# Kernel tuning notes

Hardware: AMD Instinct MI355X
Metric: run time of the kernel (lower is better)

The kernel has to match this reference:

```python
import jax, jax.numpy as jnp
import numpy as np

B_, L_, DM, DI, N_, R_ = 8, 2048, 192, 384, 16, 12  # batch, seq, d_model, d_inner, d_state, dt_rank
LN_EPS = 1e-5


def setup_inputs() -> dict:
    key = jax.random.key(0)
    ks = jax.random.split(key, 7)
    x = jax.random.normal(ks[0], (B_, L_, DM), jnp.float32)
    W_in = (jax.random.normal(ks[1], (2 * DI, DM), jnp.float32) * 0.02)
    x_proj_w = (jax.random.normal(ks[2], (R_ + 2 * N_, DI), jnp.float32) * 0.02)
    dt_std = R_ ** (-0.5)
    dt_proj_w = jax.random.uniform(ks[3], (DI, R_), jnp.float32, -dt_std, dt_std)
    # dt bias init: inverse-softplus of dt ~ LogUniform(1e-3, 1e-1)
    dt = jnp.exp(jax.random.uniform(ks[4], (DI,), jnp.float32) * (np.log(0.1) - np.log(0.001)) + np.log(0.001))
    dt = jnp.clip(dt, 1e-4, None)
    dt_proj_b = dt + jnp.log(-jnp.expm1(-dt))
    # A_log init: log(1..N) repeated over d_inner
    A_logs = jnp.log(jnp.tile(jnp.arange(1, N_ + 1, dtype=jnp.float32), (DI, 1)))  # [DI, N]
    Ds = jnp.ones((DI,), jnp.float32)
    ln_gamma = jnp.ones((DI,), jnp.float32)
    ln_beta = jnp.zeros((DI,), jnp.float32)
    W_out = (jax.random.normal(ks[5], (DM, DI), jnp.float32) * 0.02)
    return dict(x=x, W_in=W_in, x_proj_w=x_proj_w, dt_proj_w=dt_proj_w,
                dt_proj_b=dt_proj_b, A_logs=A_logs, Ds=Ds,
                ln_gamma=ln_gamma, ln_beta=ln_beta, W_out=W_out)


def _selective_scan(u, delta, A, Bs, Cs, Ds):
    # u, delta: [B, L, DI]; A: [DI, N]; Bs, Cs: [B, L, N]; Ds: [DI]
    def step(h, inp):
        d_t, u_t, B_t, C_t = inp              # [B,DI], [B,DI], [B,N], [B,N]
        dA = jnp.exp(d_t[..., None] * A)       # [B,DI,N]
        h = dA * h + (d_t * u_t)[..., None] * B_t[:, None, :]
        y_t = jnp.einsum('bdn,bn->bd', h, C_t)
        return h, y_t

    h0 = jnp.zeros((u.shape[0], u.shape[2], A.shape[1]), u.dtype)
    seq = (jnp.moveaxis(delta, 1, 0), jnp.moveaxis(u, 1, 0),
           jnp.moveaxis(Bs, 1, 0), jnp.moveaxis(Cs, 1, 0))
    _, ys = jax.lax.scan(step, h0, seq)        # ys: [L,B,DI]
    return jnp.moveaxis(ys, 0, 1) + Ds * u     # [B,L,DI]


def reference(x, W_in, x_proj_w, dt_proj_w, dt_proj_b, A_logs, Ds, ln_gamma, ln_beta, W_out):
    # in_proj + SiLU, then split into (u, z)  (d_conv <= 1 branch, non-softmax version)
    xz = jax.nn.silu(x @ W_in.T)               # [B,L,2*DI]
    u, z = jnp.split(xz, 2, axis=-1)           # [B,L,DI] each
    # x -> (dt, B, C) projections (K = 1)
    dbl = jnp.einsum('bld,cd->blc', u, x_proj_w)          # [B,L,R+2N]
    dts = dbl[..., :R_] @ dt_proj_w.T                      # [B,L,DI]
    Bs = dbl[..., R_:R_ + N_]                              # [B,L,N]
    Cs = dbl[..., R_ + N_:]                                # [B,L,N]
    delta = jax.nn.softplus(dts + dt_proj_b)               # delta_bias + softplus
    A = -jnp.exp(A_logs)                                   # [DI,N]
    y = _selective_scan(u, delta, A, Bs, Cs, Ds)           # [B,L,DI]
    # out_norm (LayerNorm over d_inner)
    mu = jnp.mean(y, axis=-1, keepdims=True)
    var = jnp.var(y, axis=-1, keepdims=True)
    y = (y - mu) * jax.lax.rsqrt(var + LN_EPS) * ln_gamma + ln_beta
    # gate and out_proj
    y = y * z
    return y @ W_out.T                                     # [B,L,DM]
```

## Files before the change

kernel.cpp:

```cpp
#include <hip/hip_runtime.h>
#include <hip/hip_bf16.h>
#include <math.h>


#define ROWS 16384
#define NCHUNK 64
#define CLEN 32

typedef short bf16x8 __attribute__((ext_vector_type(8)));
typedef float f32x4 __attribute__((ext_vector_type(4)));

__device__ __forceinline__ unsigned short f2bf(float f) {
    unsigned u = __float_as_uint(f);
    return (unsigned short)((u + 0x7fffu + ((u >> 16) & 1u)) >> 16);
}
__device__ __forceinline__ float bf2f(unsigned short h) {
    return __uint_as_float(((unsigned)h) << 16);
}

#define LOG2E 1.44269504088896f

#define LDK 40
__global__ __launch_bounds__(256) void k1_gemm_silu(
    const float* __restrict__ x, const float* __restrict__ Win,
    float* __restrict__ u, float* __restrict__ z)
{
    __shared__ short Ah[128 * LDK];
    __shared__ short Al[128 * LDK];
    __shared__ short Bh[128 * LDK];
    __shared__ short Bl[128 * LDK];
    const int tid = threadIdx.x;
    const int lane = tid & 63;
    const int w = tid >> 6;
    const int wr = w >> 1, wc = w & 1;
    const int bm = blockIdx.x * 128;
    const int bn = blockIdx.y * 128;

    f32x4 acc[4][4];
#pragma unroll
    for (int i = 0; i < 4; ++i)
#pragma unroll
        for (int j = 0; j < 4; ++j) acc[i][j] = (f32x4)0.f;

    const int r16 = lane & 15, q4 = lane >> 4;

    for (int k0 = 0; k0 < 192; k0 += 32) {
#pragma unroll
        for (int i = 0; i < 4; ++i) {
            int p = tid + i * 256;
            int r = p >> 3, k4 = (p & 7) * 4;
            float4 av = *(const float4*)(x + (size_t)(bm + r) * 192 + k0 + k4);
            unsigned short hx = f2bf(av.x), hy = f2bf(av.y), hz = f2bf(av.z), hw = f2bf(av.w);
            unsigned hi0 = (unsigned)hx | ((unsigned)hy << 16);
            unsigned hi1 = (unsigned)hz | ((unsigned)hw << 16);
            unsigned short lx = f2bf(av.x - bf2f(hx)), ly = f2bf(av.y - bf2f(hy));
            unsigned short lz = f2bf(av.z - bf2f(hz)), lw = f2bf(av.w - bf2f(hw));
            unsigned lo0 = (unsigned)lx | ((unsigned)ly << 16);
            unsigned lo1 = (unsigned)lz | ((unsigned)lw << 16);
            int wi = r * (LDK / 2) + (k4 >> 1);
            ((unsigned*)Ah)[wi] = hi0; ((unsigned*)Ah)[wi + 1] = hi1;
            ((unsigned*)Al)[wi] = lo0; ((unsigned*)Al)[wi + 1] = lo1;

            float4 bv = *(const float4*)(Win + (size_t)(bn + r) * 192 + k0 + k4);
            hx = f2bf(bv.x); hy = f2bf(bv.y); hz = f2bf(bv.z); hw = f2bf(bv.w);
            hi0 = (unsigned)hx | ((unsigned)hy << 16);
            hi1 = (unsigned)hz | ((unsigned)hw << 16);
            lx = f2bf(bv.x - bf2f(hx)); ly = f2bf(bv.y - bf2f(hy));
            lz = f2bf(bv.z - bf2f(hz)); lw = f2bf(bv.w - bf2f(hw));
            lo0 = (unsigned)lx | ((unsigned)ly << 16);
            lo1 = (unsigned)lz | ((unsigned)lw << 16);
            ((unsigned*)Bh)[wi] = hi0; ((unsigned*)Bh)[wi + 1] = hi1;
            ((unsigned*)Bl)[wi] = lo0; ((unsigned*)Bl)[wi + 1] = lo1;
        }
        __syncthreads();

        bf16x8 ah[4], al[4];
#pragma unroll
        for (int mt = 0; mt < 4; ++mt) {
            int off = (wr * 64 + mt * 16 + r16) * LDK + q4 * 8;
            ah[mt] = *(const bf16x8*)(Ah + off);
            al[mt] = *(const bf16x8*)(Al + off);
        }
#pragma unroll
        for (int nt = 0; nt < 4; ++nt) {
            int off = (wc * 64 + nt * 16 + r16) * LDK + q4 * 8;
            bf16x8 bh = *(const bf16x8*)(Bh + off);
            bf16x8 bl = *(const bf16x8*)(Bl + off);
#pragma unroll
            for (int mt = 0; mt < 4; ++mt) {
                acc[mt][nt] = __builtin_amdgcn_mfma_f32_16x16x32_bf16(ah[mt], bh, acc[mt][nt], 0, 0, 0);
                acc[mt][nt] = __builtin_amdgcn_mfma_f32_16x16x32_bf16(ah[mt], bl, acc[mt][nt], 0, 0, 0);
                acc[mt][nt] = __builtin_amdgcn_mfma_f32_16x16x32_bf16(al[mt], bh, acc[mt][nt], 0, 0, 0);
            }
        }
        __syncthreads();
    }

    float* dst = (bn < 384) ? u : z;
    const int col0 = (bn < 384) ? bn : (bn - 384);
#pragma unroll
    for (int mt = 0; mt < 4; ++mt) {
#pragma unroll
        for (int nt = 0; nt < 4; ++nt) {
            int col = col0 + wc * 64 + nt * 16 + r16;
#pragma unroll
            for (int r = 0; r < 4; ++r) {
                int row = bm + wr * 64 + mt * 16 + q4 * 4 + r;
                float s = acc[mt][nt][r];
                dst[(size_t)row * 384 + col] = s / (1.f + __expf(-s));
            }
        }
    }
}

__global__ __launch_bounds__(256) void k2_proj(
    const float* __restrict__ u, const float* __restrict__ xpw,
    const float* __restrict__ dtw, const float* __restrict__ dtb,
    float* __restrict__ delta, float* __restrict__ Bso, float* __restrict__ Cso)
{
    __shared__ float As[64 * 68];
    __shared__ float Bs[64 * 53];
    __shared__ float dtwS[384 * 13];
    __shared__ float dblS[64 * 13];
    const int tid = threadIdx.x;
    const int tx = tid & 15, ty = tid >> 4;
    const int row0 = blockIdx.x * 64;

#pragma unroll
    for (int i = 0; i < 5; ++i) {
        int p = tid + i * 256;
        if (p < 1152) {
            int dd = p / 3, q = (p % 3) * 4;
            float4 v = *(const float4*)(dtw + dd * 12 + q);
            dtwS[dd * 13 + q + 0] = v.x;
            dtwS[dd * 13 + q + 1] = v.y;
            dtwS[dd * 13 + q + 2] = v.z;
            dtwS[dd * 13 + q + 3] = v.w;
        }
    }

    float acc[4][3];
#pragma unroll
    for (int i = 0; i < 4; ++i)
#pragma unroll
        for (int g = 0; g < 3; ++g) acc[i][g] = 0.f;

    for (int k0 = 0; k0 < 384; k0 += 64) {
#pragma unroll
        for (int i = 0; i < 4; ++i) {
            int p = tid + i * 256;
            int r = p >> 4, k4 = (p & 15) * 4;
            float4 v = *(const float4*)(u + (size_t)(row0 + r) * 384 + k0 + k4);
            As[(k4 + 0) * 68 + r] = v.x;
            As[(k4 + 1) * 68 + r] = v.y;
            As[(k4 + 2) * 68 + r] = v.z;
            As[(k4 + 3) * 68 + r] = v.w;
        }
#pragma unroll
        for (int i = 0; i < 3; ++i) {
            int p = tid + i * 256;
            int c = p >> 4, k4 = (p & 15) * 4;
            float4 v = make_float4(0.f, 0.f, 0.f, 0.f);
            if (c < 44) v = *(const float4*)(xpw + (size_t)c * 384 + k0 + k4);
            Bs[(k4 + 0) * 53 + c] = v.x;
            Bs[(k4 + 1) * 53 + c] = v.y;
            Bs[(k4 + 2) * 53 + c] = v.z;
            Bs[(k4 + 3) * 53 + c] = v.w;
        }
        __syncthreads();
#pragma unroll 8
        for (int kk = 0; kk < 64; ++kk) {
            float4 a = *(const float4*)(As + kk * 68 + ty * 4);
            float b0 = Bs[kk * 53 + tx];
            float b1 = Bs[kk * 53 + tx + 16];
            float b2 = Bs[kk * 53 + tx + 32];
            acc[0][0] = fmaf(a.x, b0, acc[0][0]);
            acc[1][0] = fmaf(a.y, b0, acc[1][0]);
            acc[2][0] = fmaf(a.z, b0, acc[2][0]);
            acc[3][0] = fmaf(a.w, b0, acc[3][0]);
            acc[0][1] = fmaf(a.x, b1, acc[0][1]);
            acc[1][1] = fmaf(a.y, b1, acc[1][1]);
            acc[2][1] = fmaf(a.z, b1, acc[2][1]);
            acc[3][1] = fmaf(a.w, b1, acc[3][1]);
            acc[0][2] = fmaf(a.x, b2, acc[0][2]);
            acc[1][2] = fmaf(a.y, b2, acc[1][2]);
            acc[2][2] = fmaf(a.z, b2, acc[2][2]);
            acc[3][2] = fmaf(a.w, b2, acc[3][2]);
        }
        __syncthreads();
    }

#pragma unroll
    for (int i = 0; i < 4; ++i) {
        int lr = ty * 4 + i;
        int row = row0 + lr;
#pragma unroll
        for (int g = 0; g < 3; ++g) {
            int c = g * 16 + tx;
            float s = acc[i][g];
            if (c < 12)      dblS[lr * 13 + c] = s;
            else if (c < 28) Bso[(size_t)row * 16 + (c - 12)] = s;
            else if (c < 44) Cso[(size_t)row * 16 + (c - 28)] = s;
        }
    }
    __syncthreads();

    for (int it = 0; it < 96; ++it) {
        int o = it * 256 + tid;
        int r = o / 384, d = o - r * 384;
        float s = dtb[d];
        const float* wr = dtwS + d * 13;
        const float* db = dblS + r * 13;
#pragma unroll
        for (int j = 0; j < 12; ++j) s = fmaf(db[j], wr[j], s);
        float sp = (s > 20.f) ? s : log1pf(__expf(s));
        delta[(size_t)(row0 + r) * 384 + d] = sp;
    }
}

__global__ __launch_bounds__(384) void k3a_scan1(
    const float* __restrict__ delta, const float* __restrict__ u,
    const float* __restrict__ Bsv, const float* __restrict__ A_logs,
    float* __restrict__ hf, float* __restrict__ Ssum)
{
    const int tid = threadIdx.x;
    const int lane = tid & 63;
    const int wv = tid >> 6;
    const int c = blockIdx.x;
    const int b = blockIdx.y;
    const int d = wv * 64 + lane;
    const int t0 = c * CLEN;

    float Ac[16];
    {
#pragma unroll
        for (int q = 0; q < 4; ++q) {
            float4 v = *(const float4*)(A_logs + d * 16 + q * 4);
            Ac[q * 4 + 0] = -__expf(v.x) * LOG2E;
            Ac[q * 4 + 1] = -__expf(v.y) * LOG2E;
            Ac[q * 4 + 2] = -__expf(v.z) * LOG2E;
            Ac[q * 4 + 3] = -__expf(v.w) * LOG2E;
        }
    }

    const float* dp = delta + ((size_t)b * 2048 + t0) * 384 + d;
    const float* up = u     + ((size_t)b * 2048 + t0) * 384 + d;
    const float* Bp = Bsv   + ((size_t)b * 2048 + t0) * 16;

    float h[16];
#pragma unroll
    for (int n = 0; n < 16; ++n) h[n] = 0.f;
    float S = 0.f;

    float dv_n = dp[0], uv_n = up[0];
    float4 B0n = *(const float4*)(Bp + 0);
    float4 B1n = *(const float4*)(Bp + 4);
    float4 B2n = *(const float4*)(Bp + 8);
    float4 B3n = *(const float4*)(Bp + 12);

    for (int s = 0; s < CLEN; ++s) {
        float dv = dv_n, uv = uv_n;
        float4 B0 = B0n, B1 = B1n, B2 = B2n, B3 = B3n;
        if (s + 1 < CLEN) {
            dp += 384; up += 384; Bp += 16;
            dv_n = dp[0]; uv_n = up[0];
            B0n = *(const float4*)(Bp + 0);
            B1n = *(const float4*)(Bp + 4);
            B2n = *(const float4*)(Bp + 8);
            B3n = *(const float4*)(Bp + 12);
        }
        __builtin_amdgcn_sched_barrier(0);
        S += dv;
        float dvu = dv * uv;
        float Br[16] = {B0.x, B0.y, B0.z, B0.w, B1.x, B1.y, B1.z, B1.w,
                        B2.x, B2.y, B2.z, B2.w, B3.x, B3.y, B3.z, B3.w};
#pragma unroll
        for (int n = 0; n < 16; ++n) {
            float a = exp2f(dv * Ac[n]);
            h[n] = fmaf(a, h[n], dvu * Br[n]);
        }
    }

    const size_t ho = (((size_t)b * NCHUNK + c) * 384 + d) * 16;
#pragma unroll
    for (int q = 0; q < 4; ++q)
        *(float4*)(hf + ho + q * 4) = make_float4(h[q*4+0], h[q*4+1], h[q*4+2], h[q*4+3]);
    Ssum[((size_t)b * NCHUNK + c) * 384 + d] = S;
}

__global__ __launch_bounds__(256) void k3c_combine(
    float* __restrict__ hf, const float* __restrict__ Ssum,
    const float* __restrict__ A_logs)
{
    const int tid = threadIdx.x;
    const int n = tid & 15, dl = tid >> 4;
    const int d = blockIdx.x * 16 + dl;
    const int b = blockIdx.y;
    const float Ac = -__expf(A_logs[d * 16 + n]) * LOG2E;

    float h = 0.f;
    for (int c = 0; c < NCHUNK; ++c) {
        const size_t idx = (((size_t)b * NCHUNK + c) * 384 + d) * 16 + n;
        float hfv = hf[idx];
        float Sv  = Ssum[((size_t)b * NCHUNK + c) * 384 + d];
        hf[idx] = h;
        float P = exp2f(Ac * Sv);
        h = fmaf(P, h, hfv);
    }
}

__global__ __launch_bounds__(384) void k3b_scan2(
    float* __restrict__ dy, const float* __restrict__ u,
    const float* __restrict__ Bsv, const float* __restrict__ Csv,
    const float* __restrict__ A_logs, const float* __restrict__ Ds,
    const float* __restrict__ hf)
{
    const int tid = threadIdx.x;
    const int lane = tid & 63;
    const int wv = tid >> 6;
    const int c = blockIdx.x;
    const int b = blockIdx.y;
    const int d = wv * 64 + lane;
    const int t0 = c * CLEN;

    float Ac[16];
#pragma unroll
    for (int q = 0; q < 4; ++q) {
        float4 v = *(const float4*)(A_logs + d * 16 + q * 4);
        Ac[q * 4 + 0] = -__expf(v.x) * LOG2E;
        Ac[q * 4 + 1] = -__expf(v.y) * LOG2E;
        Ac[q * 4 + 2] = -__expf(v.z) * LOG2E;
        Ac[q * 4 + 3] = -__expf(v.w) * LOG2E;
    }
    const float Dd = Ds[d];

    float h[16];
    {
        const size_t ho = (((size_t)b * NCHUNK + c) * 384 + d) * 16;
#pragma unroll
        for (int q = 0; q < 4; ++q) {
            float4 v = *(const float4*)(hf + ho + q * 4);
            h[q * 4 + 0] = v.x; h[q * 4 + 1] = v.y;
            h[q * 4 + 2] = v.z; h[q * 4 + 3] = v.w;
        }
    }

    float* yp       = dy  + ((size_t)b * 2048 + t0) * 384 + d;
    const float* up = u   + ((size_t)b * 2048 + t0) * 384 + d;
    const float* Bp = Bsv + ((size_t)b * 2048 + t0) * 16;
    const float* Cp = Csv + ((size_t)b * 2048 + t0) * 16;

    float dv_n = yp[0], uv_n = up[0];
    float4 B0n = *(const float4*)(Bp + 0);
    float4 B1n = *(const float4*)(Bp + 4);
    float4 B2n = *(const float4*)(Bp + 8);
    float4 B3n = *(const float4*)(Bp + 12);
    float4 C0n = *(const float4*)(Cp + 0);
    float4 C1n = *(const float4*)(Cp + 4);
    float4 C2n = *(const float4*)(Cp + 8);
    float4 C3n = *(const float4*)(Cp + 12);
    const float* dpn = yp + 384;

    for (int s = 0; s < CLEN; ++s) {
        float dv = dv_n, uv = uv_n;
        float4 B0 = B0n, B1 = B1n, B2 = B2n, B3 = B3n;
        float4 C0 = C0n, C1 = C1n, C2 = C2n, C3 = C3n;
        if (s + 1 < CLEN) {
            up += 384; Bp += 16; Cp += 16;
            dv_n = dpn[0]; uv_n = up[0];
            B0n = *(const float4*)(Bp + 0);
            B1n = *(const float4*)(Bp + 4);
            B2n = *(const float4*)(Bp + 8);
            B3n = *(const float4*)(Bp + 12);
            C0n = *(const float4*)(Cp + 0);
            C1n = *(const float4*)(Cp + 4);
            C2n = *(const float4*)(Cp + 8);
            C3n = *(const float4*)(Cp + 12);
            dpn += 384;
        }
        __builtin_amdgcn_sched_barrier(0);
        float dvu = dv * uv;
        float Br[16] = {B0.x, B0.y, B0.z, B0.w, B1.x, B1.y, B1.z, B1.w,
                        B2.x, B2.y, B2.z, B2.w, B3.x, B3.y, B3.z, B3.w};
        float Cr[16] = {C0.x, C0.y, C0.z, C0.w, C1.x, C1.y, C1.z, C1.w,
                        C2.x, C2.y, C2.z, C2.w, C3.x, C3.y, C3.z, C3.w};
        float y = Dd * uv;
#pragma unroll
        for (int n = 0; n < 16; ++n) {
            float a = exp2f(dv * Ac[n]);
            h[n] = fmaf(a, h[n], dvu * Br[n]);
            y = fmaf(Cr[n], h[n], y);
        }
        yp[0] = y;
        yp += 384;
    }
}

__global__ __launch_bounds__(256) void k4_ln_mul(
    float* __restrict__ y, const float* __restrict__ z,
    const float* __restrict__ gamma, const float* __restrict__ beta)
{
    const int tid = threadIdx.x;
    const int lane = tid & 63;
    const int w = tid >> 6;
    const size_t row = (size_t)blockIdx.x * 4 + w;
    float* yr = y + row * 384;
    const float* zr = z + row * 384;
    float v[6];
    float s1 = 0.f, s2 = 0.f;
#pragma unroll
    for (int j = 0; j < 6; ++j) {
        v[j] = yr[lane + j * 64];
        s1 += v[j];
        s2 = fmaf(v[j], v[j], s2);
    }
#pragma unroll
    for (int off = 32; off > 0; off >>= 1) {
        s1 += __shfl_xor(s1, off);
        s2 += __shfl_xor(s2, off);
    }
    float mu = s1 * (1.f / 384.f);
    float var = s2 * (1.f / 384.f) - mu * mu;
    float rs = rsqrtf(var + 1e-5f);
#pragma unroll
    for (int j = 0; j < 6; ++j) {
        int d = lane + j * 64;
        float o = (v[j] - mu) * rs * gamma[d] + beta[d];
        yr[d] = o * zr[d];
    }
}

__global__ __launch_bounds__(256) void k5_gemm_out(
    const float* __restrict__ yn, const float* __restrict__ Wout,
    float* __restrict__ out)
{
    __shared__ short Ah[128 * LDK];
    __shared__ short Al[128 * LDK];
    __shared__ short Bh[64 * LDK];
    __shared__ short Bl[64 * LDK];
    const int tid = threadIdx.x;
    const int lane = tid & 63;
    const int w = tid >> 6;
    const int wr = w >> 1, wc = w & 1;
    const int bm = blockIdx.x * 128;
    const int bn = blockIdx.y * 64;

    f32x4 acc[4][2];
#pragma unroll
    for (int i = 0; i < 4; ++i)
#pragma unroll
        for (int j = 0; j < 2; ++j) acc[i][j] = (f32x4)0.f;

    const int r16 = lane & 15, q4 = lane >> 4;

    for (int k0 = 0; k0 < 384; k0 += 32) {
#pragma unroll
        for (int i = 0; i < 4; ++i) {
            int p = tid + i * 256;
            int r = p >> 3, k4 = (p & 7) * 4;
            float4 av = *(const float4*)(yn + (size_t)(bm + r) * 384 + k0 + k4);
            unsigned short hx = f2bf(av.x), hy = f2bf(av.y), hz = f2bf(av.z), hw = f2bf(av.w);
            unsigned hi0 = (unsigned)hx | ((unsigned)hy << 16);
            unsigned hi1 = (unsigned)hz | ((unsigned)hw << 16);
            unsigned short lx = f2bf(av.x - bf2f(hx)), ly = f2bf(av.y - bf2f(hy));
            unsigned short lz = f2bf(av.z - bf2f(hz)), lw = f2bf(av.w - bf2f(hw));
            unsigned lo0 = (unsigned)lx | ((unsigned)ly << 16);
            unsigned lo1 = (unsigned)lz | ((unsigned)lw << 16);
            int wi = r * (LDK / 2) + (k4 >> 1);
            ((unsigned*)Ah)[wi] = hi0; ((unsigned*)Ah)[wi + 1] = hi1;
            ((unsigned*)Al)[wi] = lo0; ((unsigned*)Al)[wi + 1] = lo1;
        }
#pragma unroll
        for (int i = 0; i < 2; ++i) {
            int p = tid + i * 256;
            int r = p >> 3, k4 = (p & 7) * 4;
            float4 bv = *(const float4*)(Wout + (size_t)(bn + r) * 384 + k0 + k4);
            unsigned short hx = f2bf(bv.x), hy = f2bf(bv.y), hz = f2bf(bv.z), hw = f2bf(bv.w);
            unsigned hi0 = (unsigned)hx | ((unsigned)hy << 16);
            unsigned hi1 = (unsigned)hz | ((unsigned)hw << 16);
            unsigned short lx = f2bf(bv.x - bf2f(hx)), ly = f2bf(bv.y - bf2f(hy));
            unsigned short lz = f2bf(bv.z - bf2f(hz)), lw = f2bf(bv.w - bf2f(hw));
            unsigned lo0 = (unsigned)lx | ((unsigned)ly << 16);
            unsigned lo1 = (unsigned)lz | ((unsigned)lw << 16);
            int wi = r * (LDK / 2) + (k4 >> 1);
            ((unsigned*)Bh)[wi] = hi0; ((unsigned*)Bh)[wi + 1] = hi1;
            ((unsigned*)Bl)[wi] = lo0; ((unsigned*)Bl)[wi + 1] = lo1;
        }
        __syncthreads();

        bf16x8 ah[4], al[4];
#pragma unroll
        for (int mt = 0; mt < 4; ++mt) {
            int off = (wr * 64 + mt * 16 + r16) * LDK + q4 * 8;
            ah[mt] = *(const bf16x8*)(Ah + off);
            al[mt] = *(const bf16x8*)(Al + off);
        }
#pragma unroll
        for (int nt = 0; nt < 2; ++nt) {
            int off = (wc * 32 + nt * 16 + r16) * LDK + q4 * 8;
            bf16x8 bh = *(const bf16x8*)(Bh + off);
            bf16x8 bl = *(const bf16x8*)(Bl + off);
#pragma unroll
            for (int mt = 0; mt < 4; ++mt) {
                acc[mt][nt] = __builtin_amdgcn_mfma_f32_16x16x32_bf16(ah[mt], bh, acc[mt][nt], 0, 0, 0);
                acc[mt][nt] = __builtin_amdgcn_mfma_f32_16x16x32_bf16(ah[mt], bl, acc[mt][nt], 0, 0, 0);
                acc[mt][nt] = __builtin_amdgcn_mfma_f32_16x16x32_bf16(al[mt], bh, acc[mt][nt], 0, 0, 0);
            }
        }
        __syncthreads();
    }

#pragma unroll
    for (int mt = 0; mt < 4; ++mt) {
#pragma unroll
        for (int nt = 0; nt < 2; ++nt) {
            int col = bn + wc * 32 + nt * 16 + r16;
#pragma unroll
            for (int r = 0; r < 4; ++r) {
                int row = bm + wr * 64 + mt * 16 + q4 * 4 + r;
                out[(size_t)row * 192 + col] = acc[mt][nt][r];
            }
        }
    }
}

extern "C" void kernel_launch(void* const* d_in, const int* in_sizes, int n_in,
                              void* d_out, int out_size, void* d_ws, size_t ws_size,
                              hipStream_t stream) {
    const float* x    = (const float*)d_in[0];
    const float* Win  = (const float*)d_in[1];
    const float* xpw  = (const float*)d_in[2];
    const float* dtw  = (const float*)d_in[3];
    const float* dtb  = (const float*)d_in[4];
    const float* Alog = (const float*)d_in[5];
    const float* Dsv  = (const float*)d_in[6];
    const float* lng  = (const float*)d_in[7];
    const float* lnb  = (const float*)d_in[8];
    const float* Wout = (const float*)d_in[9];
    float* out = (float*)d_out;

    const size_t nU  = (size_t)ROWS * 384;
    const size_t nBC = (size_t)ROWS * 16;
    const size_t nHF = (size_t)8 * NCHUNK * 384 * 16;
    const size_t nS  = (size_t)8 * NCHUNK * 384;
    const size_t need = (nU * 3 + nBC * 2 + nHF + nS) * sizeof(float);
    if (ws_size < need) return;

    float* u    = (float*)d_ws;
    float* z    = u + nU;
    float* dl   = z + nU;
    float* Bsv  = dl + nU;
    float* Csv  = Bsv + nBC;
    float* hf   = Csv + nBC;
    float* Ssum = hf + nHF;

    k1_gemm_silu<<<dim3(128, 6), 256, 0, stream>>>(x, Win, u, z);
    k2_proj<<<256, 256, 0, stream>>>(u, xpw, dtw, dtb, dl, Bsv, Csv);
    k3a_scan1<<<dim3(NCHUNK, 8), 384, 0, stream>>>(dl, u, Bsv, Alog, hf, Ssum);
    k3c_combine<<<dim3(24, 8), 256, 0, stream>>>(hf, Ssum, Alog);
    k3b_scan2<<<dim3(NCHUNK, 8), 384, 0, stream>>>(dl, u, Bsv, Csv, Alog, Dsv, hf);
    k4_ln_mul<<<4096, 256, 0, stream>>>(dl, z, lng, lnb);
    k5_gemm_out<<<dim3(128, 3), 256, 0, stream>>>(dl, Wout, out);
}
```

Measured before the change: 300.9 us.

## Use split-bf16 MFMA with register prefetch for x_proj GEMM in k2_proj

```diff
diff --git a/kernel.cpp b/kernel.cpp
--- a/kernel.cpp
+++ b/kernel.cpp
@@ -113,17 +113,22 @@
     }
 }
 
+#define LDK2 72
 __global__ __launch_bounds__(256) void k2_proj(
     const float* __restrict__ u, const float* __restrict__ xpw,
     const float* __restrict__ dtw, const float* __restrict__ dtb,
     float* __restrict__ delta, float* __restrict__ Bso, float* __restrict__ Cso)
 {
-    __shared__ float As[64 * 68];
-    __shared__ float Bs[64 * 53];
+    __shared__ __align__(16) short Ah[64 * LDK2];
+    __shared__ __align__(16) short Al[64 * LDK2];
+    __shared__ __align__(16) short Bh[48 * LDK2];
+    __shared__ __align__(16) short Bl[48 * LDK2];
     __shared__ float dtwS[384 * 13];
     __shared__ float dblS[64 * 13];
     const int tid = threadIdx.x;
-    const int tx = tid & 15, ty = tid >> 4;
+    const int lane = tid & 63;
+    const int w = tid >> 6;
+    const int r16 = lane & 15, q4 = lane >> 4;
     const int row0 = blockIdx.x * 64;
 
 #pragma unroll
@@ -139,65 +144,100 @@
         }
     }
 
-    float acc[4][3];
-#pragma unroll
-    for (int i = 0; i < 4; ++i)
-#pragma unroll
-        for (int g = 0; g < 3; ++g) acc[i][g] = 0.f;
-
-    for (int k0 = 0; k0 < 384; k0 += 64) {
+    f32x4 acc[3];
+#pragma unroll
+    for (int j = 0; j < 3; ++j) acc[j] = (f32x4)0.f;
+
+    float4 aReg[4], bReg[3];
+#pragma unroll
+    for (int i = 0; i < 4; ++i) {
+        int p = tid + i * 256;
+        int r = p >> 4, k4 = (p & 15) * 4;
+        aReg[i] = *(const float4*)(u + (size_t)(row0 + r) * 384 + k4);
+    }
+#pragma unroll
+    for (int i = 0; i < 3; ++i) {
+        int p = tid + i * 256;
+        int c = p >> 4, k4 = (p & 15) * 4;
+        bReg[i] = (c < 44) ? *(const float4*)(xpw + (size_t)c * 384 + k4)
+                           : make_float4(0.f, 0.f, 0.f, 0.f);
+    }
+
+    for (int ck = 0; ck < 6; ++ck) {
 #pragma unroll
         for (int i = 0; i < 4; ++i) {
             int p = tid + i * 256;
             int r = p >> 4, k4 = (p & 15) * 4;
-            float4 v = *(const float4*)(u + (size_t)(row0 + r) * 384 + k0 + k4);
-            As[(k4 + 0) * 68 + r] = v.x;
-            As[(k4 + 1) * 68 + r] = v.y;
-            As[(k4 + 2) * 68 + r] = v.z;
-            As[(k4 + 3) * 68 + r] = v.w;
+            float4 av = aReg[i];
+            unsigned short hx = f2bf(av.x), hy = f2bf(av.y), hz = f2bf(av.z), hw = f2bf(av.w);
+            unsigned short lx = f2bf(av.x - bf2f(hx)), ly = f2bf(av.y - bf2f(hy));
+            unsigned short lz = f2bf(av.z - bf2f(hz)), lw = f2bf(av.w - bf2f(hw));
+            int wi = r * (LDK2 / 2) + (k4 >> 1);
+            ((unsigned*)Ah)[wi]     = (unsigned)hx | ((unsigned)hy << 16);
+            ((unsigned*)Ah)[wi + 1] = (unsigned)hz | ((unsigned)hw << 16);
+            ((unsigned*)Al)[wi]     = (unsigned)lx | ((unsigned)ly << 16);
+            ((unsigned*)Al)[wi + 1] = (unsigned)lz | ((unsigned)lw << 16);
         }
 #pragma unroll
         for (int i = 0; i < 3; ++i) {
             int p = tid + i * 256;
             int c = p >> 4, k4 = (p & 15) * 4;
-            float4 v = make_float4(0.f, 0.f, 0.f, 0.f);
-            if (c < 44) v = *(const float4*)(xpw + (size_t)c * 384 + k0 + k4);
-            Bs[(k4 + 0) * 53 + c] = v.x;
-            Bs[(k4 + 1) * 53 + c] = v.y;
-            Bs[(k4 + 2) * 53 + c] = v.z;
-            Bs[(k4 + 3) * 53 + c] = v.w;
+            float4 bv = bReg[i];
+            unsigned short hx = f2bf(bv.x), hy = f2bf(bv.y), hz = f2bf(bv.z), hw = f2bf(bv.w);
+            unsigned short lx = f2bf(bv.x - bf2f(hx)), ly = f2bf(bv.y - bf2f(hy));
+            unsigned short lz = f2bf(bv.z - bf2f(hz)), lw = f2bf(bv.w - bf2f(hw));
+            int wi = c * (LDK2 / 2) + (k4 >> 1);
+            ((unsigned*)Bh)[wi]     = (unsigned)hx | ((unsigned)hy << 16);
+            ((unsigned*)Bh)[wi + 1] = (unsigned)hz | ((unsigned)hw << 16);
+            ((unsigned*)Bl)[wi]     = (unsigned)lx | ((unsigned)ly << 16);
+            ((unsigned*)Bl)[wi + 1] = (unsigned)lz | ((unsigned)lw << 16);
         }
         __syncthreads();
-#pragma unroll 8
-        for (int kk = 0; kk < 64; ++kk) {
-            float4 a = *(const float4*)(As + kk * 68 + ty * 4);
-            float b0 = Bs[kk * 53 + tx];
-            float b1 = Bs[kk * 53 + tx + 16];
-            float b2 = Bs[kk * 53 + tx + 32];
-            acc[0][0] = fmaf(a.x, b0, acc[0][0]);
-            acc[1][0] = fmaf(a.y, b0, acc[1][0]);
-            acc[2][0] = fmaf(a.z, b0, acc[2][0]);
-            acc[3][0] = fmaf(a.w, b0, acc[3][0]);
-            acc[0][1] = fmaf(a.x, b1, acc[0][1]);
-            acc[1][1] = fmaf(a.y, b1, acc[1][1]);
-            acc[2][1] = fmaf(a.z, b1, acc[2][1]);
-            acc[3][1] = fmaf(a.w, b1, acc[3][1]);
-            acc[0][2] = fmaf(a.x, b2, acc[0][2]);
-            acc[1][2] = fmaf(a.y, b2, acc[1][2]);
-            acc[2][2] = fmaf(a.z, b2, acc[2][2]);
-            acc[3][2] = fmaf(a.w, b2, acc[3][2]);
+
+        if (ck + 1 < 6) {
+            int k0 = (ck + 1) * 64;
+#pragma unroll
+            for (int i = 0; i < 4; ++i) {
+                int p = tid + i * 256;
+                int r = p >> 4, k4 = (p & 15) * 4;
+                aReg[i] = *(const float4*)(u + (size_t)(row0 + r) * 384 + k0 + k4);
+            }
+#pragma unroll
+            for (int i = 0; i < 3; ++i) {
+                int p = tid + i * 256;
+                int c = p >> 4, k4 = (p & 15) * 4;
+                bReg[i] = (c < 44) ? *(const float4*)(xpw + (size_t)c * 384 + k0 + k4)
+                                   : make_float4(0.f, 0.f, 0.f, 0.f);
+            }
+        }
+        __builtin_amdgcn_sched_barrier(0);
+
+#pragma unroll
+        for (int ks = 0; ks < 2; ++ks) {
+            int aoff = (w * 16 + r16) * LDK2 + ks * 32 + q4 * 8;
+            bf16x8 ah = *(const bf16x8*)(Ah + aoff);
+            bf16x8 al = *(const bf16x8*)(Al + aoff);
+#pragma unroll
+            for (int nt = 0; nt < 3; ++nt) {
+                int boff = (nt * 16 + r16) * LDK2 + ks * 32 + q4 * 8;
+                bf16x8 bh = *(const bf16x8*)(Bh + boff);
+                bf16x8 bl = *(const bf16x8*)(Bl + boff);
+                acc[nt] = __builtin_amdgcn_mfma_f32_16x16x32_bf16(ah, bh, acc[nt], 0, 0, 0);
+                acc[nt] = __builtin_amdgcn_mfma_f32_16x16x32_bf16(ah, bl, acc[nt], 0, 0, 0);
+                acc[nt] = __builtin_amdgcn_mfma_f32_16x16x32_bf16(al, bh, acc[nt], 0, 0, 0);
+            }
         }
         __syncthreads();
     }
 
 #pragma unroll
-    for (int i = 0; i < 4; ++i) {
-        int lr = ty * 4 + i;
-        int row = row0 + lr;
-#pragma unroll
-        for (int g = 0; g < 3; ++g) {
-            int c = g * 16 + tx;
-            float s = acc[i][g];
+    for (int nt = 0; nt < 3; ++nt) {
+        int c = nt * 16 + r16;
+#pragma unroll
+        for (int r = 0; r < 4; ++r) {
+            int lr = w * 16 + q4 * 4 + r;
+            int row = row0 + lr;
+            float s = acc[nt][r];
             if (c < 12)      dblS[lr * 13 + c] = s;
             else if (c < 28) Bso[(size_t)row * 16 + (c - 12)] = s;
             else if (c < 44) Cso[(size_t)row * 16 + (c - 28)] = s;
```

New measurement: 295.3 us. About the same (-1.9%).

## Rewrite x_proj GEMM in k2 with split-bf16 MFMA and split-K reduction

Applied to the files above, without the earlier changes.

```diff
diff --git a/kernel.cpp b/kernel.cpp
--- a/kernel.cpp
+++ b/kernel.cpp
@@ -17,8 +17,27 @@
 __device__ __forceinline__ float bf2f(unsigned short h) {
     return __uint_as_float(((unsigned)h) << 16);
 }
+__device__ __forceinline__ void cvt8(float4 a0, float4 a1, bf16x8& hi, bf16x8& lo) {
+    float v[8] = {a0.x, a0.y, a0.z, a0.w, a1.x, a1.y, a1.z, a1.w};
+#pragma unroll
+    for (int j = 0; j < 8; ++j) {
+        unsigned short h = f2bf(v[j]);
+        hi[j] = (short)h;
+        lo[j] = (short)f2bf(v[j] - bf2f(h));
+    }
+}
 
 #define LOG2E 1.44269504088896f
+
+__global__ __launch_bounds__(384) void k0_split(
+    const float* __restrict__ xpw, short* __restrict__ xpwH, short* __restrict__ xpwL)
+{
+    const int c = blockIdx.x, k = threadIdx.x;
+    float v = (c < 44) ? xpw[(size_t)c * 384 + k] : 0.f;
+    unsigned short h = f2bf(v);
+    xpwH[(size_t)c * 384 + k] = (short)h;
+    xpwL[(size_t)c * 384 + k] = (short)f2bf(v - bf2f(h));
+}
 
 #define LDK 40
 __global__ __launch_bounds__(256) void k1_gemm_silu(
@@ -113,106 +132,88 @@
     }
 }
 
-__global__ __launch_bounds__(256) void k2_proj(
-    const float* __restrict__ u, const float* __restrict__ xpw,
+__global__ __launch_bounds__(384) void k2_proj(
+    const float* __restrict__ u, const short* __restrict__ xpwH,
+    const short* __restrict__ xpwL,
     const float* __restrict__ dtw, const float* __restrict__ dtb,
     float* __restrict__ delta, float* __restrict__ Bso, float* __restrict__ Cso)
 {
-    __shared__ float As[64 * 68];
-    __shared__ float Bs[64 * 53];
-    __shared__ float dtwS[384 * 13];
-    __shared__ float dblS[64 * 13];
-    const int tid = threadIdx.x;
-    const int tx = tid & 15, ty = tid >> 4;
-    const int row0 = blockIdx.x * 64;
-
-#pragma unroll
-    for (int i = 0; i < 5; ++i) {
-        int p = tid + i * 256;
-        if (p < 1152) {
-            int dd = p / 3, q = (p % 3) * 4;
-            float4 v = *(const float4*)(dtw + dd * 12 + q);
-            dtwS[dd * 13 + q + 0] = v.x;
-            dtwS[dd * 13 + q + 1] = v.y;
-            dtwS[dd * 13 + q + 2] = v.z;
-            dtwS[dd * 13 + q + 3] = v.w;
-        }
-    }
-
-    float acc[4][3];
-#pragma unroll
-    for (int i = 0; i < 4; ++i)
-#pragma unroll
-        for (int g = 0; g < 3; ++g) acc[i][g] = 0.f;
-
-    for (int k0 = 0; k0 < 384; k0 += 64) {
-#pragma unroll
-        for (int i = 0; i < 4; ++i) {
-            int p = tid + i * 256;
-            int r = p >> 4, k4 = (p & 15) * 4;
-            float4 v = *(const float4*)(u + (size_t)(row0 + r) * 384 + k0 + k4);
-            As[(k4 + 0) * 68 + r] = v.x;
-            As[(k4 + 1) * 68 + r] = v.y;
-            As[(k4 + 2) * 68 + r] = v.z;
-            As[(k4 + 3) * 68 + r] = v.w;
-        }
-#pragma unroll
-        for (int i = 0; i < 3; ++i) {
-            int p = tid + i * 256;
-            int c = p >> 4, k4 = (p & 15) * 4;
-            float4 v = make_float4(0.f, 0.f, 0.f, 0.f);
-            if (c < 44) v = *(const float4*)(xpw + (size_t)c * 384 + k0 + k4);
-            Bs[(k4 + 0) * 53 + c] = v.x;
-            Bs[(k4 + 1) * 53 + c] = v.y;
-            Bs[(k4 + 2) * 53 + c] = v.z;
-            Bs[(k4 + 3) * 53 + c] = v.w;
-        }
-        __syncthreads();
-#pragma unroll 8
-        for (int kk = 0; kk < 64; ++kk) {
-            float4 a = *(const float4*)(As + kk * 68 + ty * 4);
-            float b0 = Bs[kk * 53 + tx];
-            float b1 = Bs[kk * 53 + tx + 16];
-            float b2 = Bs[kk * 53 + tx + 32];
-            acc[0][0] = fmaf(a.x, b0, acc[0][0]);
-            acc[1][0] = fmaf(a.y, b0, acc[1][0]);
-            acc[2][0] = fmaf(a.z, b0, acc[2][0]);
-            acc[3][0] = fmaf(a.w, b0, acc[3][0]);
-            acc[0][1] = fmaf(a.x, b1, acc[0][1]);
-            acc[1][1] = fmaf(a.y, b1, acc[1][1]);
-            acc[2][1] = fmaf(a.z, b1, acc[2][1]);
-            acc[3][1] = fmaf(a.w, b1, acc[3][1]);
-            acc[0][2] = fmaf(a.x, b2, acc[0][2]);
-            acc[1][2] = fmaf(a.y, b2, acc[1][2]);
-            acc[2][2] = fmaf(a.z, b2, acc[2][2]);
-            acc[3][2] = fmaf(a.w, b2, acc[3][2]);
-        }
-        __syncthreads();
-    }
-
-#pragma unroll
-    for (int i = 0; i < 4; ++i) {
-        int lr = ty * 4 + i;
-        int row = row0 + lr;
-#pragma unroll
-        for (int g = 0; g < 3; ++g) {
-            int c = g * 16 + tx;
-            float s = acc[i][g];
-            if (c < 12)      dblS[lr * 13 + c] = s;
-            else if (c < 28) Bso[(size_t)row * 16 + (c - 12)] = s;
-            else if (c < 44) Cso[(size_t)row * 16 + (c - 28)] = s;
-        }
+    __shared__ float red[2][2][16][49];
+    __shared__ float dblS[32 * 13];
+    const int tid = threadIdx.x;
+    const int lane = tid & 63;
+    const int w = tid >> 6;
+    const int mt = w & 1, ks = w >> 1;
+    const int r16 = lane & 15, q4 = lane >> 4;
+    const int row0 = blockIdx.x * 32;
+    const int arow = row0 + mt * 16 + r16;
+
+    f32x4 acc[3];
+#pragma unroll
+    for (int j = 0; j < 3; ++j) acc[j] = (f32x4)0.f;
+
+#pragma unroll
+    for (int ck = 0; ck < 4; ++ck) {
+        const int kb = ks * 128 + ck * 32 + q4 * 8;
+        const float* ap = u + (size_t)arow * 384 + kb;
+        float4 a0 = *(const float4*)(ap);
+        float4 a1 = *(const float4*)(ap + 4);
+        bf16x8 ah, al;
+        cvt8(a0, a1, ah, al);
+#pragma unroll
+        for (int nt = 0; nt < 3; ++nt) {
+            const int col = nt * 16 + r16;
+            bf16x8 bh = *(const bf16x8*)(xpwH + (size_t)col * 384 + kb);
+            bf16x8 bl = *(const bf16x8*)(xpwL + (size_t)col * 384 + kb);
+            acc[nt] = __builtin_amdgcn_mfma_f32_16x16x32_bf16(ah, bh, acc[nt], 0, 0, 0);
+            acc[nt] = __builtin_amdgcn_mfma_f32_16x16x32_bf16(ah, bl, acc[nt], 0, 0, 0);
+            acc[nt] = __builtin_amdgcn_mfma_f32_16x16x32_bf16(al, bh, acc[nt], 0, 0, 0);
+        }
+    }
+
+    if (ks > 0) {
+#pragma unroll
+        for (int nt = 0; nt < 3; ++nt)
+#pragma unroll
+            for (int r = 0; r < 4; ++r)
+                red[ks - 1][mt][q4 * 4 + r][nt * 16 + r16] = acc[nt][r];
     }
     __syncthreads();
-
-    for (int it = 0; it < 96; ++it) {
-        int o = it * 256 + tid;
-        int r = o / 384, d = o - r * 384;
-        float s = dtb[d];
-        const float* wr = dtwS + d * 13;
+    if (ks == 0) {
+#pragma unroll
+        for (int nt = 0; nt < 3; ++nt)
+#pragma unroll
+            for (int r = 0; r < 4; ++r)
+                acc[nt][r] += red[0][mt][q4 * 4 + r][nt * 16 + r16]
+                            + red[1][mt][q4 * 4 + r][nt * 16 + r16];
+
+#pragma unroll
+        for (int nt = 0; nt < 3; ++nt) {
+            int c = nt * 16 + r16;
+#pragma unroll
+            for (int r = 0; r < 4; ++r) {
+                int lr = mt * 16 + q4 * 4 + r;
+                int row = row0 + lr;
+                float s = acc[nt][r];
+                if (c < 12)      dblS[lr * 13 + c] = s;
+                else if (c < 28) Bso[(size_t)row * 16 + (c - 12)] = s;
+                else if (c < 44) Cso[(size_t)row * 16 + (c - 28)] = s;
+            }
+        }
+    }
+    __syncthreads();
+
+    const int d = tid;
+    float wr_[12];
+#pragma unroll
+    for (int j = 0; j < 12; ++j) wr_[j] = dtw[(size_t)d * 12 + j];
+    const float bias = dtb[d];
+#pragma unroll 4
+    for (int r = 0; r < 32; ++r) {
         const float* db = dblS + r * 13;
-#pragma unroll
-        for (int j = 0; j < 12; ++j) s = fmaf(db[j], wr[j], s);
+        float s = bias;
+#pragma unroll
+        for (int j = 0; j < 12; ++j) s = fmaf(db[j], wr_[j], s);
         float sp = (s > 20.f) ? s : log1pf(__expf(s));
         delta[(size_t)(row0 + r) * 384 + d] = sp;
     }
@@ -543,7 +544,8 @@
     const size_t nBC = (size_t)ROWS * 16;
     const size_t nHF = (size_t)8 * NCHUNK * 384 * 16;
     const size_t nS  = (size_t)8 * NCHUNK * 384;
-    const size_t need = (nU * 3 + nBC * 2 + nHF + nS) * sizeof(float);
+    const size_t nXW = (size_t)48 * 384;
+    const size_t need = (nU * 3 + nBC * 2 + nHF + nS) * sizeof(float) + nXW * 2 * sizeof(short);
     if (ws_size < need) return;
 
     float* u    = (float*)d_ws;
@@ -553,9 +555,12 @@
     float* Csv  = Bsv + nBC;
     float* hf   = Csv + nBC;
     float* Ssum = hf + nHF;
-
+    short* xpwH = (short*)(Ssum + nS);
+    short* xpwL = xpwH + nXW;
+
+    k0_split<<<48, 384, 0, stream>>>(xpw, xpwH, xpwL);
     k1_gemm_silu<<<dim3(128, 6), 256, 0, stream>>>(x, Win, u, z);
-    k2_proj<<<256, 256, 0, stream>>>(u, xpw, dtw, dtb, dl, Bsv, Csv);
+    k2_proj<<<512, 384, 0, stream>>>(u, xpwH, xpwL, dtw, dtb, dl, Bsv, Csv);
     k3a_scan1<<<dim3(NCHUNK, 8), 384, 0, stream>>>(dl, u, Bsv, Alog, hf, Ssum);
     k3c_combine<<<dim3(24, 8), 256, 0, stream>>>(hf, Ssum, Alog);
     k3b_scan2<<<dim3(NCHUNK, 8), 384, 0, stream>>>(dl, u, Bsv, Csv, Alog, Dsv, hf);
```

Result: faster. 276.6 us (-8.1%).
